# Kernel tuning notes

Hardware: AMD Instinct MI355X
Metric: run time of the kernel (lower is better)

## Reference

```python
import jax, jax.numpy as jnp
import numpy as np
from jax import lax

COCO_80_TO_91 = [1,2,3,4,5,6,7,8,9,10,11,13,14,15,16,17,18,19,20,21,22,23,24,25,27,28,31,32,33,34,35,36,37,38,39,40,41,42,43,44,46,47,48,49,50,51,52,53,54,55,56,57,58,59,60,61,62,63,64,65,67,70,72,73,74,75,76,77,78,79,80,81,82,84,85,86,87,88,89,90]

CONF = 0.25      # self.confidence
IOU_THR = 0.7    # ultralytics NMS default
TOPK = 1000      # candidate cap before NMS
MAX_DET = 300    # ultralytics max_det default
MAX_WH = 7680.0  # per-class offset trick
IMG_SZ = 640.0   # yolov8 letterboxed input size


def setup_inputs() -> dict:
    key = jax.random.key(0)
    preds = jax.random.uniform(key, (32, 84, 8400), dtype=jnp.float32)
    return {"preds": preds}


def _nms_single(boxes, scores):
    """Greedy NMS on score-descending boxes [K,4] (class-offset xyxy). Returns keep mask [K]."""
    K = boxes.shape[0]
    area = (boxes[:, 2] - boxes[:, 0]) * (boxes[:, 3] - boxes[:, 1])  # [K]
    lt = jnp.maximum(boxes[:, None, :2], boxes[None, :, :2])          # [K,K,2]
    rb = jnp.minimum(boxes[:, None, 2:], boxes[None, :, 2:])
    wh = jnp.clip(rb - lt, 0.0)
    inter = wh[..., 0] * wh[..., 1]
    iou = inter / (area[:, None] + area[None, :] - inter + 1e-7)       # [K,K]
    idx = jnp.arange(K)
    sup = (iou > IOU_THR) & (idx[None, :] > idx[:, None])              # i suppresses later j

    def body(i, keep):
        return jnp.where(keep[i], keep & ~sup[i], keep)

    return lax.fori_loop(0, K, body, jnp.ones((K,), dtype=bool))


def reference(preds):
    # preds: [B, 84, N] -> [B, N, 84]
    p = jnp.transpose(preds, (0, 2, 1))
    box_xywh = p[..., :4] * IMG_SZ           # xywh in pixels on 640x640 canvas
    cls = p[..., 4:]                          # [B, N, 80]
    scores = jnp.max(cls, axis=-1)            # best-class confidence
    labels = jnp.argmax(cls, axis=-1)         # 0..79
    xy, wh = box_xywh[..., :2], box_xywh[..., 2:]
    xyxy = jnp.concatenate([xy - wh * 0.5, xy + wh * 0.5], axis=-1)  # decode

    # confidence filter + top-K candidate selection (score-descending)
    s_masked = jnp.where(scores > CONF, scores, -1.0)
    top_s, top_i = lax.top_k(s_masked, TOPK)                          # [B,TOPK]
    top_b = jnp.take_along_axis(xyxy, top_i[..., None], axis=1)      # [B,TOPK,4]
    top_l = jnp.take_along_axis(labels, top_i, axis=1)               # [B,TOPK]

    # per-class NMS via class offset
    off_b = top_b + (top_l.astype(top_b.dtype) * MAX_WH)[..., None]
    keep = jax.vmap(_nms_single)(off_b, top_s) & (top_s > CONF)

    # select final max_det detections, zero-pad invalid slots
    fin_s = jnp.where(keep, top_s, -1.0)
    out_s, out_i = lax.top_k(fin_s, MAX_DET)                          # [B,MAX_DET]
    out_b = jnp.take_along_axis(top_b, out_i[..., None], axis=1)
    out_l = jnp.take_along_axis(top_l, out_i, axis=1)
    valid = out_s > CONF
    boxes = jnp.where(valid[..., None], out_b, 0.0)
    scores_out = jnp.where(valid, out_s, 0.0)
    mapped = jnp.asarray(COCO_80_TO_91, dtype=jnp.int64)[out_l]       # COCO 80 -> 91 ids
    labels_out = jnp.where(valid, mapped, 0)
    return boxes, scores_out, labels_out
```

## Files before the change

kernel.cpp:

```cpp
#include <hip/hip_runtime.h>
#include <stdint.h>

typedef unsigned long long u64;
typedef unsigned int u32;

#define BATCH 32
#define NCH 84
#define NA 8400
#define NCLS 80
#define TOPK 1000
#define MAXDET 300
#define CONF 0.25f
#define IOU_T 0.7f
#define MAX_WH 7680.0f
#define IMG_SZ 640.0f
#define NT 1024
#define KPT 9
#define NCOPY 8
#define HPAD 260

__device__ __constant__ float coco_map_f[NCLS] = {
    1,2,3,4,5,6,7,8,9,10,11,13,14,15,16,17,18,19,20,21,22,23,24,25,27,28,
    31,32,33,34,35,36,37,38,39,40,41,42,43,44,46,47,48,49,50,51,52,53,54,
    55,56,57,58,59,60,61,62,63,64,65,67,70,72,73,74,75,76,77,78,79,80,81,
    82,84,85,86,87,88,89,90};

__device__ inline u64 shflx64(u64 v, int m) {
    int lo = __shfl_xor((int)(u32)(v & 0xFFFFFFFFull), m, 64);
    int hi = __shfl_xor((int)(u32)(v >> 32), m, 64);
    return ((u64)(u32)hi << 32) | (u32)lo;
}

__global__ __launch_bounds__(256)
void decode_kernel(const float* __restrict__ preds,
                   u64* __restrict__ keys,
                   float4* __restrict__ boxes) {
    const int b = blockIdx.y;
    const int a = blockIdx.x * 256 + threadIdx.x;
    const bool live = (a < NA);
    const int ac = live ? a : (NA - 1);
    const float* p = preds + (size_t)b * NCH * NA + ac;

    float bx = p[0];
    float by = p[(size_t)1 * NA];
    float bw = p[(size_t)2 * NA];
    float bh = p[(size_t)3 * NA];

    const float* pc = p + (size_t)4 * NA;
    float best = -1.0f;
    int bl = 0;
#pragma unroll 16
    for (int r = 0; r < NCLS; ++r) {
        float v = pc[(size_t)r * NA];
        bl = (v > best) ? r : bl;
        best = fmaxf(v, best);
    }

    if (live) {
        float fx = bx * IMG_SZ, fy = by * IMG_SZ;
        float fw = bw * IMG_SZ, fh = bh * IMG_SZ;
        float hw = fw * 0.5f, hh = fh * 0.5f;
        boxes[(size_t)b * NA + a] = make_float4(fx - hw, fy - hh, fx + hw, fy + hh);
        float s = (best > CONF) ? best : -1.0f;
        u32 fb = __float_as_uint(s);
        u32 u = (fb & 0x80000000u) ? ~fb : (fb | 0x80000000u);
        keys[(size_t)b * NA + a] =
            ((u64)u << 21) | ((u64)(16383 - a) << 7) | (u64)bl;
    }
}

__global__ __launch_bounds__(NT, 4)
void select_sort_kernel(const u64* __restrict__ keys,
                        const float4* __restrict__ boxes,
                        u64* __restrict__ sortedk,
                        float4* __restrict__ gbox,
                        float4* __restrict__ goffb,
                        float* __restrict__ garea,
                        unsigned short* __restrict__ grank,
                        int* __restrict__ gccnt) {
    const int b = blockIdx.x;
    const int t = threadIdx.x;
    const int lane = t & 63, wid = t >> 6;

    __shared__ union {
        struct {
            u64 sk[2][NT];
            int hist[NCOPY * HPAD];
        } a;
        struct {
            u64 cmask2[NCLS][16];
        } bb;
    } u_s;
    __shared__ int selB, selK, hselS, smax, scnt, cnt_s;

    u64 kreg[KPT];
    const u64* kb = keys + (size_t)b * NA;
#pragma unroll
    for (int j = 0; j < KPT; ++j) {
        int i = t + j * NT;
        kreg[j] = (i < NA) ? kb[i] : 0ull;
    }

    u64 P = 0ull;
    int kk = TOPK;
    int nsel = 0;
    for (int d = 3; d >= 0; --d) {
        const int sh = 21 + 8 * d;
        __syncthreads();
        if (t == 0) { smax = -1; scnt = 0; }
        __syncthreads();
        u64 hmask = (~0ull) << (sh + 8);
        int dig[KPT];
        int mymax = -1;
#pragma unroll
        for (int j = 0; j < KPT; ++j) {
            bool act = (((kreg[j] ^ P) & hmask) == 0ull) && (kreg[j] != 0ull);
            dig[j] = act ? (int)((kreg[j] >> sh) & 255) : -1;
            mymax = max(mymax, dig[j]);
        }
#pragma unroll
        for (int off = 32; off; off >>= 1)
            mymax = max(mymax, __shfl_down(mymax, off, 64));
        if (lane == 0) atomicMax(&smax, mymax);
        __syncthreads();
        int maxb = smax;
        int myc = 0;
#pragma unroll
        for (int j = 0; j < KPT; ++j) myc += (dig[j] == maxb) ? 1 : 0;
#pragma unroll
        for (int off = 32; off; off >>= 1) myc += __shfl_down(myc, off, 64);
        if (lane == 0) atomicAdd(&scnt, myc);
        __syncthreads();
        int cm = scnt;
        if (cm >= kk) {
            P |= ((u64)maxb) << sh;
            nsel = TOPK - kk + cm;
            if (nsel <= NT) break;
            continue;
        }
        for (int i = t; i < NCOPY * HPAD; i += NT) u_s.a.hist[i] = 0;
        __syncthreads();
        int* myh = u_s.a.hist + (wid & (NCOPY - 1)) * HPAD;
#pragma unroll
        for (int j = 0; j < KPT; ++j)
            if (dig[j] >= 0) atomicAdd(&myh[dig[j]], 1);
        __syncthreads();
        if (t < 64) {
            int h0 = 0, h1 = 0, h2 = 0, h3 = 0;
            for (int c = 0; c < NCOPY; ++c) {
                const int* hp = u_s.a.hist + c * HPAD + 4 * t;
                h0 += hp[0]; h1 += hp[1]; h2 += hp[2]; h3 += hp[3];
            }
            int s = h0 + h1 + h2 + h3;
            int S = s;
            #pragma unroll
            for (int off = 1; off < 64; off <<= 1) {
                int o = __shfl_down(S, off, 64);
                if (t + off < 64) S += o;
            }
            int Snext = S - s;
            int c3 = Snext + h3, c2 = c3 + h2, c1 = c2 + h1, c0 = c1 + h0;
            int cand = -1, above = 0;
            if (c0 >= kk) {
                if      (c3 >= kk) { cand = 4 * t + 3; above = Snext; }
                else if (c2 >= kk) { cand = 4 * t + 2; above = c3; }
                else if (c1 >= kk) { cand = 4 * t + 1; above = c2; }
                else               { cand = 4 * t;     above = c1; }
            }
            int pc = (cand < 0) ? 0 : (((cand + 1) << 16) | (kk - above));
            #pragma unroll
            for (int off = 32; off; off >>= 1)
                pc = max(pc, __shfl_down(pc, off, 64));
            pc = __shfl(pc, 0, 64);
            int B = (pc >> 16) - 1;
            if (t == (B >> 2)) {
                int m4 = B & 3;
                selB = B;
                selK = pc & 0xFFFF;
                hselS = (m4 == 0) ? h0 : (m4 == 1) ? h1 : (m4 == 2) ? h2 : h3;
            }
        }
        __syncthreads();
        P |= ((u64)selB) << sh;
        kk = selK;
        nsel = TOPK - kk + hselS;
        if (nsel <= NT) break;
    }

    __syncthreads();
    if (t == 0) cnt_s = 0;
    __syncthreads();
#pragma unroll
    for (int j = 0; j < KPT; ++j) {
        bool p = (kreg[j] >= P);
        u64 m = __ballot(p);
        int base = 0;
        if (lane == 0) base = atomicAdd(&cnt_s, (int)__popcll(m));
        base = __shfl(base, 0, 64);
        if (p) {
            int pos = base + (int)__popcll(m & ((1ull << lane) - 1ull));
            if (pos < NT) u_s.a.sk[0][pos] = kreg[j];
        }
    }
    if (t < NT - nsel) u_s.a.sk[0][nsel + t] = 0ull;
    __syncthreads();

    u64 myk = u_s.a.sk[0][t];
    int buf = 1;
    for (int size = 2; size <= NT; size <<= 1) {
        bool up = ((t & size) == 0);
        for (int stride = size >> 1; stride; stride >>= 1) {
            u64 pk;
            if (stride >= 64) {
                u_s.a.sk[buf][t] = myk;
                __syncthreads();
                pk = u_s.a.sk[buf][t ^ stride];
                buf ^= 1;
            } else {
                pk = shflx64(myk, stride);
            }
            bool tlow = ((t & stride) == 0);
            u64 mn = (myk < pk) ? myk : pk;
            u64 mx = (myk < pk) ? pk : myk;
            myk = up ? (tlow ? mx : mn) : (tlow ? mn : mx);
        }
    }
    sortedk[(size_t)b * NT + t] = myk;

    __syncthreads();
    for (int i = t; i < NCLS * 16; i += NT) ((u64*)u_s.bb.cmask2)[i] = 0ull;
    __syncthreads();

    int my_L = 0;
    float4 bx = make_float4(0.f, 0.f, 0.f, 0.f);
    if (t < TOPK) {
        int my_a = 16383 - (int)((myk >> 7) & 16383ull);
        my_L = (int)(myk & 127ull);
        bx = boxes[(size_t)b * NA + my_a];
        atomicOr(&u_s.bb.cmask2[my_L][t >> 6], 1ull << (t & 63));
    }
    __syncthreads();
    if (t < TOPK) {
        int w = t >> 6;
        int r = __popcll(u_s.bb.cmask2[my_L][w] & ((1ull << (t & 63)) - 1ull));
        for (int q = 0; q < w; ++q) r += __popcll(u_s.bb.cmask2[my_L][q]);
        gbox[(size_t)b * NT + t] = bx;
        if (r < 64) {
            float off = (float)my_L * MAX_WH;
            float ox0 = bx.x + off, oy0 = bx.y + off;
            float ox1 = bx.z + off, oy1 = bx.w + off;
            size_t ci = ((size_t)b * NCLS + my_L) * 64 + r;
            goffb[ci] = make_float4(ox0, oy0, ox1, oy1);
            garea[ci] = (ox1 - ox0) * (oy1 - oy0);
            grank[ci] = (unsigned short)t;
        }
    }
    if (t < NCLS) {
        int s = 0;
#pragma unroll
        for (int q = 0; q < 16; ++q) s += __popcll(u_s.bb.cmask2[t][q]);
        gccnt[(size_t)b * NCLS + t] = s;
    }
}

__global__ __launch_bounds__(64)
void nms_kernel(const float4* __restrict__ goffb,
                const float* __restrict__ garea,
                const unsigned short* __restrict__ grank,
                const int* __restrict__ gccnt,
                const u64* __restrict__ sortedk,
                const float4* __restrict__ gbox,
                unsigned char* __restrict__ keepg) {
    const int c = blockIdx.x;
    const int b = blockIdx.y;
    const int lane = threadIdx.x;
    const int n = gccnt[(size_t)b * NCLS + c];
    if (n == 0) return;

    if (n <= 64) {
        size_t ci = ((size_t)b * NCLS + c) * 64 + lane;
        float4 bb = make_float4(0.f, 0.f, 0.f, 0.f);
        float ar = 0.f;
        int rk = 0;
        if (lane < n) { bb = goffb[ci]; ar = garea[ci]; rk = grank[ci]; }
        u64 colm = 0ull;
        for (int i = 0; i < n; ++i) {
            float hx0 = __shfl(bb.x, i, 64);
            float hy0 = __shfl(bb.y, i, 64);
            float hx1 = __shfl(bb.z, i, 64);
            float hy1 = __shfl(bb.w, i, 64);
            float ha  = __shfl(ar, i, 64);
            float lx = fmaxf(hx0, bb.x), ly = fmaxf(hy0, bb.y);
            float rx = fminf(hx1, bb.z), ry = fminf(hy1, bb.w);
            float w = fmaxf(rx - lx, 0.0f);
            float h = fmaxf(ry - ly, 0.0f);
            float inter = w * h;
            float denom = ha + ar;
            denom = denom - inter;
            denom = denom + 1e-7f;
            bool s = (lane > i) && (lane < n) && (inter / denom > IOU_T);
            colm |= ((u64)s) << i;
        }
        u64 alive = (n >= 64) ? ~0ull : ((1ull << n) - 1ull);
        for (int i = 0; i < n; ++i) {
            if (!((alive >> i) & 1ull)) continue;
            alive &= ~__ballot((colm >> i) & 1ull);
        }
        if (lane < n) keepg[(size_t)b * NT + rk] = (unsigned char)((alive >> lane) & 1ull);
    } else if (lane == 0) {
        const u64* skb = sortedk + (size_t)b * NT;
        const float4* gb = gbox + (size_t)b * NT;
        const float off = (float)c * MAX_WH;
        u64 aliveW[16];
        for (int q = 0; q < 16; ++q) aliveW[q] = ~0ull;
        for (int i = 0; i < TOPK; ++i) {
            if ((int)(skb[i] & 127ull) != c) continue;
            if (!((aliveW[i >> 6] >> (i & 63)) & 1ull)) continue;
            float4 g = gb[i];
            float ix0 = g.x + off, iy0 = g.y + off;
            float ix1 = g.z + off, iy1 = g.w + off;
            float ai = (ix1 - ix0) * (iy1 - iy0);
            for (int jj = i + 1; jj < TOPK; ++jj) {
                if ((int)(skb[jj] & 127ull) != c) continue;
                if (!((aliveW[jj >> 6] >> (jj & 63)) & 1ull)) continue;
                float4 h = gb[jj];
                float jx0 = h.x + off, jy0 = h.y + off;
                float jx1 = h.z + off, jy1 = h.w + off;
                float aj = (jx1 - jx0) * (jy1 - jy0);
                float lx = fmaxf(ix0, jx0), ly = fmaxf(iy0, jy0);
                float rx = fminf(ix1, jx1), ry = fminf(iy1, jy1);
                float ww = fmaxf(rx - lx, 0.0f);
                float hh = fmaxf(ry - ly, 0.0f);
                float inter = ww * hh;
                float denom = ai + aj;
                denom = denom - inter;
                denom = denom + 1e-7f;
                if (inter / denom > IOU_T) aliveW[jj >> 6] &= ~(1ull << (jj & 63));
            }
        }
        for (int i = 0; i < TOPK; ++i)
            if ((int)(skb[i] & 127ull) == c)
                keepg[(size_t)b * NT + i] = (unsigned char)((aliveW[i >> 6] >> (i & 63)) & 1ull);
    }
}

__global__ __launch_bounds__(NT)
void epilogue_kernel(const u64* __restrict__ sortedk,
                     const unsigned char* __restrict__ keepg,
                     const float4* __restrict__ gbox,
                     float* __restrict__ out) {
    const int b = blockIdx.x;
    const int t = threadIdx.x;
    const int lane = t & 63, wid = t >> 6;
    __shared__ int wsum[16], woff[16], ktot_s;

    u64 myk = sortedk[(size_t)b * NT + t];
    bool valid = false;
    float sj = 0.0f;
    if (t < TOPK) {
        u32 u = (u32)(myk >> 21);
        u32 fb = (u & 0x80000000u) ? (u ^ 0x80000000u) : ~u;
        sj = __uint_as_float(fb);
        valid = keepg[(size_t)b * NT + t] && (sj > CONF);
    }
    u64 m = __ballot(valid);
    if (lane == 0) wsum[wid] = (int)__popcll(m);
    __syncthreads();
    if (wid == 0) {
        int v = (lane < 16) ? wsum[lane] : 0;
        #pragma unroll
        for (int off = 1; off < 16; off <<= 1) {
            int o = __shfl_up(v, off, 64);
            if (lane >= off) v += o;
        }
        if (lane < 16) woff[lane] = v - wsum[lane];
        if (lane == 15) ktot_s = v;
    }
    __syncthreads();
    int ktot = ktot_s;
    int rank = woff[wid] + (int)__popcll(m & ((1ull << lane) - 1ull));

    float* out_boxes = out;
    float* out_scores = out + (size_t)BATCH * MAXDET * 4;
    float* out_labels = out + (size_t)BATCH * MAXDET * 5;
    if (valid && rank < MAXDET) {
        float4 bx = gbox[(size_t)b * NT + t];
        float* ob = out_boxes + ((size_t)b * MAXDET + rank) * 4;
        ob[0] = bx.x; ob[1] = bx.y; ob[2] = bx.z; ob[3] = bx.w;
        out_scores[(size_t)b * MAXDET + rank] = sj;
        out_labels[(size_t)b * MAXDET + rank] = coco_map_f[(int)(myk & 127ull)];
    }
    if (t < MAXDET && t >= ktot) {
        float* ob = out_boxes + ((size_t)b * MAXDET + t) * 4;
        ob[0] = 0.0f; ob[1] = 0.0f; ob[2] = 0.0f; ob[3] = 0.0f;
        out_scores[(size_t)b * MAXDET + t] = 0.0f;
        out_labels[(size_t)b * MAXDET + t] = 0.0f;
    }
}

extern "C" void kernel_launch(void* const* d_in, const int* in_sizes, int n_in,
                              void* d_out, int out_size, void* d_ws, size_t ws_size,
                              hipStream_t stream) {
    const float* preds = (const float*)d_in[0];
    char* ws = (char*)d_ws;
    size_t off = 0;
    auto alloc = [&](size_t bytes) { char* p = ws + off; off += (bytes + 255) & ~(size_t)255; return p; };

    u64* keys            = (u64*)           alloc((size_t)BATCH * NA * 8);
    float4* boxes        = (float4*)        alloc((size_t)BATCH * NA * 16);
    u64* sortedk         = (u64*)           alloc((size_t)BATCH * NT * 8);
    float4* gbox         = (float4*)        alloc((size_t)BATCH * NT * 16);
    float4* goffb        = (float4*)        alloc((size_t)BATCH * NCLS * 64 * 16);
    float* garea         = (float*)         alloc((size_t)BATCH * NCLS * 64 * 4);
    unsigned short* grank= (unsigned short*)alloc((size_t)BATCH * NCLS * 64 * 2);
    int* gccnt           = (int*)           alloc((size_t)BATCH * NCLS * 4);
    unsigned char* keepg = (unsigned char*) alloc((size_t)BATCH * NT);
    float* out = (float*)d_out;

    dim3 dgrid((NA + 255) / 256, BATCH);
    decode_kernel<<<dgrid, 256, 0, stream>>>(preds, keys, boxes);
    select_sort_kernel<<<BATCH, NT, 0, stream>>>(keys, boxes, sortedk, gbox,
                                                 goffb, garea, grank, gccnt);
    dim3 ngrid(NCLS, BATCH);
    nms_kernel<<<ngrid, 64, 0, stream>>>(goffb, garea, grank, gccnt,
                                         sortedk, gbox, keepg);
    epilogue_kernel<<<BATCH, NT, 0, stream>>>(sortedk, keepg, gbox, out);
}
```

Before: 164.2 us.

## Fuse per-class NMS into epilogue kernel and speed up radix select

Merges the per-class NMS kernel into the epilogue, so each batch block handles all 80 classes across its 16 waves and keeps the keep mask in shared memory instead of global memory. This removes one kernel launch and the global keepg round trip. The top-K radix select now starts with a 16-bit first digit and uses per-wave shared arrays in place of shared atomics, cutting the number of barrier-heavy passes. The trade-off is parallelism: NMS now runs on 32 blocks instead of 2560, and each wave processes five classes in sequence.

```diff
diff --git a/kernel.cpp b/kernel.cpp
--- a/kernel.cpp
+++ b/kernel.cpp
@@ -91,7 +91,8 @@
             u64 cmask2[NCLS][16];
         } bb;
     } u_s;
-    __shared__ int selB, selK, hselS, smax, scnt, cnt_s;
+    __shared__ int selB, selK, hselS, cnt_s;
+    __shared__ int wsum[16], woff[16];
 
     u64 kreg[KPT];
     const u64* kb = keys + (size_t)b * NA;
@@ -104,87 +105,128 @@
     u64 P = 0ull;
     int kk = TOPK;
     int nsel = 0;
-    for (int d = 3; d >= 0; --d) {
-        const int sh = 21 + 8 * d;
-        __syncthreads();
-        if (t == 0) { smax = -1; scnt = 0; }
-        __syncthreads();
-        u64 hmask = (~0ull) << (sh + 8);
-        int dig[KPT];
+    bool done = false;
+    bool did16 = false;
+
+    {
+        int dg[KPT];
         int mymax = -1;
 #pragma unroll
         for (int j = 0; j < KPT; ++j) {
-            bool act = (((kreg[j] ^ P) & hmask) == 0ull) && (kreg[j] != 0ull);
-            dig[j] = act ? (int)((kreg[j] >> sh) & 255) : -1;
-            mymax = max(mymax, dig[j]);
+            dg[j] = (kreg[j] != 0ull) ? (int)((kreg[j] >> 37) & 0xFFFF) : -1;
+            mymax = max(mymax, dg[j]);
         }
 #pragma unroll
         for (int off = 32; off; off >>= 1)
             mymax = max(mymax, __shfl_down(mymax, off, 64));
-        if (lane == 0) atomicMax(&smax, mymax);
+        if (lane == 0) wsum[wid] = mymax;
         __syncthreads();
-        int maxb = smax;
+        int maxd = wsum[0];
+#pragma unroll
+        for (int q = 1; q < 16; ++q) maxd = max(maxd, wsum[q]);
         int myc = 0;
 #pragma unroll
-        for (int j = 0; j < KPT; ++j) myc += (dig[j] == maxb) ? 1 : 0;
+        for (int j = 0; j < KPT; ++j) myc += (dg[j] == maxd) ? 1 : 0;
 #pragma unroll
         for (int off = 32; off; off >>= 1) myc += __shfl_down(myc, off, 64);
-        if (lane == 0) atomicAdd(&scnt, myc);
+        if (lane == 0) woff[wid] = myc;
         __syncthreads();
-        int cm = scnt;
+        int cm = 0;
+#pragma unroll
+        for (int q = 0; q < 16; ++q) cm += woff[q];
         if (cm >= kk) {
-            P |= ((u64)maxb) << sh;
-            nsel = TOPK - kk + cm;
+            P = ((u64)maxd) << 37;
+            nsel = cm;
+            did16 = true;
+            done = (nsel <= NT);
+        }
+    }
+
+    if (!done) {
+        const int dstart = did16 ? 1 : 3;
+        for (int d = dstart; d >= 0; --d) {
+            const int sh = 21 + 8 * d;
+            const u64 hmask = (~0ull) << (sh + 8);
+            int dig[KPT];
+            int mymax = -1;
+#pragma unroll
+            for (int j = 0; j < KPT; ++j) {
+                bool act = (((kreg[j] ^ P) & hmask) == 0ull) && (kreg[j] != 0ull);
+                dig[j] = act ? (int)((kreg[j] >> sh) & 255) : -1;
+                mymax = max(mymax, dig[j]);
+            }
+#pragma unroll
+            for (int off = 32; off; off >>= 1)
+                mymax = max(mymax, __shfl_down(mymax, off, 64));
+            if (lane == 0) wsum[wid] = mymax;
+            __syncthreads();
+            int maxb = wsum[0];
+#pragma unroll
+            for (int q = 1; q < 16; ++q) maxb = max(maxb, wsum[q]);
+            int myc = 0;
+#pragma unroll
+            for (int j = 0; j < KPT; ++j) myc += (dig[j] == maxb) ? 1 : 0;
+#pragma unroll
+            for (int off = 32; off; off >>= 1) myc += __shfl_down(myc, off, 64);
+            if (lane == 0) woff[wid] = myc;
+            __syncthreads();
+            int cm = 0;
+#pragma unroll
+            for (int q = 0; q < 16; ++q) cm += woff[q];
+            if (cm >= kk) {
+                P |= ((u64)maxb) << sh;
+                nsel = TOPK - kk + cm;
+                if (nsel <= NT) break;
+                continue;
+            }
+            for (int i = t; i < NCOPY * HPAD; i += NT) u_s.a.hist[i] = 0;
+            __syncthreads();
+            int* myh = u_s.a.hist + (wid & (NCOPY - 1)) * HPAD;
+#pragma unroll
+            for (int j = 0; j < KPT; ++j)
+                if (dig[j] >= 0) atomicAdd(&myh[dig[j]], 1);
+            __syncthreads();
+            if (t < 64) {
+                int h0 = 0, h1 = 0, h2 = 0, h3 = 0;
+                for (int c = 0; c < NCOPY; ++c) {
+                    const int* hp = u_s.a.hist + c * HPAD + 4 * t;
+                    h0 += hp[0]; h1 += hp[1]; h2 += hp[2]; h3 += hp[3];
+                }
+                int s = h0 + h1 + h2 + h3;
+                int S = s;
+                #pragma unroll
+                for (int off = 1; off < 64; off <<= 1) {
+                    int o = __shfl_down(S, off, 64);
+                    if (t + off < 64) S += o;
+                }
+                int Snext = S - s;
+                int c3 = Snext + h3, c2 = c3 + h2, c1 = c2 + h1, c0 = c1 + h0;
+                int cand = -1, above = 0;
+                if (c0 >= kk) {
+                    if      (c3 >= kk) { cand = 4 * t + 3; above = Snext; }
+                    else if (c2 >= kk) { cand = 4 * t + 2; above = c3; }
+                    else if (c1 >= kk) { cand = 4 * t + 1; above = c2; }
+                    else               { cand = 4 * t;     above = c1; }
+                }
+                int pc = (cand < 0) ? 0 : (((cand + 1) << 16) | (kk - above));
+                #pragma unroll
+                for (int off = 32; off; off >>= 1)
+                    pc = max(pc, __shfl_down(pc, off, 64));
+                pc = __shfl(pc, 0, 64);
+                int B = (pc >> 16) - 1;
+                if (t == (B >> 2)) {
+                    int m4 = B & 3;
+                    selB = B;
+                    selK = pc & 0xFFFF;
+                    hselS = (m4 == 0) ? h0 : (m4 == 1) ? h1 : (m4 == 2) ? h2 : h3;
+                }
+            }
+            __syncthreads();
+            P |= ((u64)selB) << sh;
+            kk = selK;
+            nsel = TOPK - kk + hselS;
             if (nsel <= NT) break;
-            continue;
-        }
-        for (int i = t; i < NCOPY * HPAD; i += NT) u_s.a.hist[i] = 0;
-        __syncthreads();
-        int* myh = u_s.a.hist + (wid & (NCOPY - 1)) * HPAD;
-#pragma unroll
-        for (int j = 0; j < KPT; ++j)
-            if (dig[j] >= 0) atomicAdd(&myh[dig[j]], 1);
-        __syncthreads();
-        if (t < 64) {
-            int h0 = 0, h1 = 0, h2 = 0, h3 = 0;
-            for (int c = 0; c < NCOPY; ++c) {
-                const int* hp = u_s.a.hist + c * HPAD + 4 * t;
-                h0 += hp[0]; h1 += hp[1]; h2 += hp[2]; h3 += hp[3];
-            }
-            int s = h0 + h1 + h2 + h3;
-            int S = s;
-            #pragma unroll
-            for (int off = 1; off < 64; off <<= 1) {
-                int o = __shfl_down(S, off, 64);
-                if (t + off < 64) S += o;
-            }
-            int Snext = S - s;
-            int c3 = Snext + h3, c2 = c3 + h2, c1 = c2 + h1, c0 = c1 + h0;
-            int cand = -1, above = 0;
-            if (c0 >= kk) {
-                if      (c3 >= kk) { cand = 4 * t + 3; above = Snext; }
-                else if (c2 >= kk) { cand = 4 * t + 2; above = c3; }
-                else if (c1 >= kk) { cand = 4 * t + 1; above = c2; }
-                else               { cand = 4 * t;     above = c1; }
-            }
-            int pc = (cand < 0) ? 0 : (((cand + 1) << 16) | (kk - above));
-            #pragma unroll
-            for (int off = 32; off; off >>= 1)
-                pc = max(pc, __shfl_down(pc, off, 64));
-            pc = __shfl(pc, 0, 64);
-            int B = (pc >> 16) - 1;
-            if (t == (B >> 2)) {
-                int m4 = B & 3;
-                selB = B;
-                selK = pc & 0xFFFF;
-                hselS = (m4 == 0) ? h0 : (m4 == 1) ? h1 : (m4 == 2) ? h2 : h3;
-            }
-        }
-        __syncthreads();
-        P |= ((u64)selB) << sh;
-        kk = selK;
-        nsel = TOPK - kk + hselS;
-        if (nsel <= NT) break;
+        }
     }
 
     __syncthreads();
@@ -263,105 +305,110 @@
     }
 }
 
-__global__ __launch_bounds__(64)
-void nms_kernel(const float4* __restrict__ goffb,
-                const float* __restrict__ garea,
-                const unsigned short* __restrict__ grank,
-                const int* __restrict__ gccnt,
-                const u64* __restrict__ sortedk,
-                const float4* __restrict__ gbox,
-                unsigned char* __restrict__ keepg) {
-    const int c = blockIdx.x;
-    const int b = blockIdx.y;
-    const int lane = threadIdx.x;
-    const int n = gccnt[(size_t)b * NCLS + c];
-    if (n == 0) return;
-
-    if (n <= 64) {
-        size_t ci = ((size_t)b * NCLS + c) * 64 + lane;
-        float4 bb = make_float4(0.f, 0.f, 0.f, 0.f);
-        float ar = 0.f;
-        int rk = 0;
-        if (lane < n) { bb = goffb[ci]; ar = garea[ci]; rk = grank[ci]; }
-        u64 colm = 0ull;
-        for (int i = 0; i < n; ++i) {
-            float hx0 = __shfl(bb.x, i, 64);
-            float hy0 = __shfl(bb.y, i, 64);
-            float hx1 = __shfl(bb.z, i, 64);
-            float hy1 = __shfl(bb.w, i, 64);
-            float ha  = __shfl(ar, i, 64);
-            float lx = fmaxf(hx0, bb.x), ly = fmaxf(hy0, bb.y);
-            float rx = fminf(hx1, bb.z), ry = fminf(hy1, bb.w);
-            float w = fmaxf(rx - lx, 0.0f);
-            float h = fmaxf(ry - ly, 0.0f);
-            float inter = w * h;
-            float denom = ha + ar;
-            denom = denom - inter;
-            denom = denom + 1e-7f;
-            bool s = (lane > i) && (lane < n) && (inter / denom > IOU_T);
-            colm |= ((u64)s) << i;
-        }
-        u64 alive = (n >= 64) ? ~0ull : ((1ull << n) - 1ull);
-        for (int i = 0; i < n; ++i) {
-            if (!((alive >> i) & 1ull)) continue;
-            alive &= ~__ballot((colm >> i) & 1ull);
-        }
-        if (lane < n) keepg[(size_t)b * NT + rk] = (unsigned char)((alive >> lane) & 1ull);
-    } else if (lane == 0) {
-        const u64* skb = sortedk + (size_t)b * NT;
-        const float4* gb = gbox + (size_t)b * NT;
-        const float off = (float)c * MAX_WH;
-        u64 aliveW[16];
-        for (int q = 0; q < 16; ++q) aliveW[q] = ~0ull;
-        for (int i = 0; i < TOPK; ++i) {
-            if ((int)(skb[i] & 127ull) != c) continue;
-            if (!((aliveW[i >> 6] >> (i & 63)) & 1ull)) continue;
-            float4 g = gb[i];
-            float ix0 = g.x + off, iy0 = g.y + off;
-            float ix1 = g.z + off, iy1 = g.w + off;
-            float ai = (ix1 - ix0) * (iy1 - iy0);
-            for (int jj = i + 1; jj < TOPK; ++jj) {
-                if ((int)(skb[jj] & 127ull) != c) continue;
-                if (!((aliveW[jj >> 6] >> (jj & 63)) & 1ull)) continue;
-                float4 h = gb[jj];
-                float jx0 = h.x + off, jy0 = h.y + off;
-                float jx1 = h.z + off, jy1 = h.w + off;
-                float aj = (jx1 - jx0) * (jy1 - jy0);
-                float lx = fmaxf(ix0, jx0), ly = fmaxf(iy0, jy0);
-                float rx = fminf(ix1, jx1), ry = fminf(iy1, jy1);
-                float ww = fmaxf(rx - lx, 0.0f);
-                float hh = fmaxf(ry - ly, 0.0f);
-                float inter = ww * hh;
-                float denom = ai + aj;
-                denom = denom - inter;
-                denom = denom + 1e-7f;
-                if (inter / denom > IOU_T) aliveW[jj >> 6] &= ~(1ull << (jj & 63));
-            }
-        }
-        for (int i = 0; i < TOPK; ++i)
-            if ((int)(skb[i] & 127ull) == c)
-                keepg[(size_t)b * NT + i] = (unsigned char)((aliveW[i >> 6] >> (i & 63)) & 1ull);
-    }
-}
-
 __global__ __launch_bounds__(NT)
-void epilogue_kernel(const u64* __restrict__ sortedk,
-                     const unsigned char* __restrict__ keepg,
-                     const float4* __restrict__ gbox,
-                     float* __restrict__ out) {
+void nms_epi_kernel(const float4* __restrict__ goffb,
+                    const float* __restrict__ garea,
+                    const unsigned short* __restrict__ grank,
+                    const int* __restrict__ gccnt,
+                    const u64* __restrict__ sortedk,
+                    const float4* __restrict__ gbox,
+                    float* __restrict__ out) {
     const int b = blockIdx.x;
     const int t = threadIdx.x;
     const int lane = t & 63, wid = t >> 6;
+
+    __shared__ unsigned char keep[NT];
     __shared__ int wsum[16], woff[16], ktot_s;
 
+    keep[t] = 0;
+
+    int cnts[5];
+#pragma unroll
+    for (int j = 0; j < 5; ++j)
+        cnts[j] = gccnt[(size_t)b * NCLS + wid + 16 * j];
+
     u64 myk = sortedk[(size_t)b * NT + t];
+    __syncthreads();
+
+    for (int j = 0; j < 5; ++j) {
+        const int cc = wid + 16 * j;
+        const int n = cnts[j];
+        if (n == 0) continue;
+        if (n <= 64) {
+            size_t ci = ((size_t)b * NCLS + cc) * 64 + lane;
+            float4 bb = make_float4(0.f, 0.f, 0.f, 0.f);
+            float ar = 0.f;
+            int rk = 0;
+            if (lane < n) { bb = goffb[ci]; ar = garea[ci]; rk = grank[ci]; }
+            u64 colm = 0ull;
+            for (int i = 0; i < n; ++i) {
+                float hx0 = __shfl(bb.x, i, 64);
+                float hy0 = __shfl(bb.y, i, 64);
+                float hx1 = __shfl(bb.z, i, 64);
+                float hy1 = __shfl(bb.w, i, 64);
+                float ha  = __shfl(ar, i, 64);
+                float lx = fmaxf(hx0, bb.x), ly = fmaxf(hy0, bb.y);
+                float rx = fminf(hx1, bb.z), ry = fminf(hy1, bb.w);
+                float w = fmaxf(rx - lx, 0.0f);
+                float h = fmaxf(ry - ly, 0.0f);
+                float inter = w * h;
+                float denom = ha + ar;
+                denom = denom - inter;
+                denom = denom + 1e-7f;
+                bool s = (lane > i) && (lane < n) && (inter / denom > IOU_T);
+                colm |= ((u64)s) << i;
+            }
+            u64 alive = (n >= 64) ? ~0ull : ((1ull << n) - 1ull);
+            for (int i = 0; i < n; ++i) {
+                if (!((alive >> i) & 1ull)) continue;
+                alive &= ~__ballot((colm >> i) & 1ull);
+            }
+            if (lane < n) keep[rk] = (unsigned char)((alive >> lane) & 1ull);
+        } else if (lane == 0) {
+            const u64* skb = sortedk + (size_t)b * NT;
+            const float4* gb = gbox + (size_t)b * NT;
+            const float off = (float)cc * MAX_WH;
+            u64 aliveW[16];
+            for (int q = 0; q < 16; ++q) aliveW[q] = ~0ull;
+            for (int i = 0; i < TOPK; ++i) {
+                if ((int)(skb[i] & 127ull) != cc) continue;
+                if (!((aliveW[i >> 6] >> (i & 63)) & 1ull)) continue;
+                float4 g = gb[i];
+                float ix0 = g.x + off, iy0 = g.y + off;
+                float ix1 = g.z + off, iy1 = g.w + off;
+                float ai = (ix1 - ix0) * (iy1 - iy0);
+                for (int jj = i + 1; jj < TOPK; ++jj) {
+                    if ((int)(skb[jj] & 127ull) != cc) continue;
+                    if (!((aliveW[jj >> 6] >> (jj & 63)) & 1ull)) continue;
+                    float4 h = gb[jj];
+                    float jx0 = h.x + off, jy0 = h.y + off;
+                    float jx1 = h.z + off, jy1 = h.w + off;
+                    float aj = (jx1 - jx0) * (jy1 - jy0);
+                    float lx = fmaxf(ix0, jx0), ly = fmaxf(iy0, jy0);
+                    float rx = fminf(ix1, jx1), ry = fminf(iy1, jy1);
+                    float ww = fmaxf(rx - lx, 0.0f);
+                    float hh = fmaxf(ry - ly, 0.0f);
+                    float inter = ww * hh;
+                    float denom = ai + aj;
+                    denom = denom - inter;
+                    denom = denom + 1e-7f;
+                    if (inter / denom > IOU_T) aliveW[jj >> 6] &= ~(1ull << (jj & 63));
+                }
+            }
+            for (int i = 0; i < TOPK; ++i)
+                if ((int)(skb[i] & 127ull) == cc)
+                    keep[i] = (unsigned char)((aliveW[i >> 6] >> (i & 63)) & 1ull);
+        }
+    }
+    __syncthreads();
+
+    float sj = 0.0f;
     bool valid = false;
-    float sj = 0.0f;
     if (t < TOPK) {
         u32 u = (u32)(myk >> 21);
         u32 fb = (u & 0x80000000u) ? (u ^ 0x80000000u) : ~u;
         sj = __uint_as_float(fb);
-        valid = keepg[(size_t)b * NT + t] && (sj > CONF);
+        valid = keep[t] && (sj > CONF);
     }
     u64 m = __ballot(valid);
     if (lane == 0) wsum[wid] = (int)__popcll(m);
@@ -369,9 +416,9 @@
     if (wid == 0) {
         int v = (lane < 16) ? wsum[lane] : 0;
         #pragma unroll
-        for (int off = 1; off < 16; off <<= 1) {
-            int o = __shfl_up(v, off, 64);
-            if (lane >= off) v += o;
+        for (int o = 1; o < 16; o <<= 1) {
+            int x = __shfl_up(v, o, 64);
+            if (lane >= o) v += x;
         }
         if (lane < 16) woff[lane] = v - wsum[lane];
         if (lane == 15) ktot_s = v;
@@ -414,15 +461,12 @@
     float* garea         = (float*)         alloc((size_t)BATCH * NCLS * 64 * 4);
     unsigned short* grank= (unsigned short*)alloc((size_t)BATCH * NCLS * 64 * 2);
     int* gccnt           = (int*)           alloc((size_t)BATCH * NCLS * 4);
-    unsigned char* keepg = (unsigned char*) alloc((size_t)BATCH * NT);
     float* out = (float*)d_out;
 
     dim3 dgrid((NA + 255) / 256, BATCH);
     decode_kernel<<<dgrid, 256, 0, stream>>>(preds, keys, boxes);
     select_sort_kernel<<<BATCH, NT, 0, stream>>>(keys, boxes, sortedk, gbox,
                                                  goffb, garea, grank, gccnt);
-    dim3 ngrid(NCLS, BATCH);
-    nms_kernel<<<ngrid, 64, 0, stream>>>(goffb, garea, grank, gccnt,
-                                         sortedk, gbox, keepg);
-    epilogue_kernel<<<BATCH, NT, 0, stream>>>(sortedk, keepg, gbox, out);
+    nms_epi_kernel<<<BATCH, NT, 0, stream>>>(goffb, garea, grank, gccnt,
+                                             sortedk, gbox, out);
 }
```

Result: slower. 182.2 us (+11.0%).
